# Kernel optimization log

Hardware: AMD Instinct MI355X
Metric: run time of the kernel (lower is better)

Reference implementation:

```python
import jax, jax.numpy as jnp
import numpy as np

NUM_SAMPLES = 512
FG_FRACTION = 0.25
MAX_POS = int(NUM_SAMPLES * FG_FRACTION)  # 128
THRESHOLDS = np.array([0.0, 0.5, 0.5], dtype=np.float32)
INDICATORS = np.array([-3, -1, -2, 1], dtype=np.int32)


def _make_boxes(key, shape, scale):
    # random valid boxes: sorted corner pairs in [0, scale)
    y = jnp.sort(jax.random.uniform(key, shape[:-1] + (2,)) * scale, axis=-1)
    x = jnp.sort(jax.random.uniform(jax.random.fold_in(key, 1), shape[:-1] + (2,)) * scale, axis=-1)
    return jnp.stack([y[..., 0], x[..., 0], y[..., 1], x[..., 1]], axis=-1)


def setup_inputs() -> dict:
    key = jax.random.key(0)
    k1, k2, k3, k4 = jax.random.split(key, 4)
    B, N, M = 32, 8000, 256
    boxes = _make_boxes(k1, (B, N, 4), 1024.0)
    gt_boxes = _make_boxes(k2, (B, M, 4), 1024.0)
    # pad last quarter of gt entries with -1 (invalid)
    valid = (jnp.arange(M) < (3 * M) // 4)[None, :, None]
    gt_boxes = jnp.where(valid, gt_boxes, -jnp.ones_like(gt_boxes))
    gt_classes = jax.random.randint(k3, (B, M), 1, 91, dtype=jnp.int32)
    gt_classes = jnp.where(valid[..., 0], gt_classes, -1)
    rand = jax.random.uniform(k4, (B, N + M))
    return {"boxes": boxes, "gt_boxes": gt_boxes, "gt_classes": gt_classes, "rand": rand}


def _pairwise_iou(b1, b2):
    # b1: [B,N,4], b2: [B,M,4] in (ymin,xmin,ymax,xmax) -> [B,N,M]
    ymin1, xmin1, ymax1, xmax1 = jnp.split(b1, 4, axis=-1)  # each [B,N,1]
    ymin2, xmin2, ymax2, xmax2 = (t[..., 0] for t in jnp.split(b2, 4, axis=-1))  # [B,M]
    ih = jnp.clip(jnp.minimum(ymax1, ymax2[:, None, :]) - jnp.maximum(ymin1, ymin2[:, None, :]), 0.0)
    iw = jnp.clip(jnp.minimum(xmax1, xmax2[:, None, :]) - jnp.maximum(xmin1, xmin2[:, None, :]), 0.0)
    inter = ih * iw
    a1 = (ymax1 - ymin1) * (xmax1 - xmin1)          # [B,N,1]
    a2 = (ymax2 - ymin2) * (xmax2 - xmin2)          # [B,M]
    union = a1 + a2[:, None, :] - inter
    return jnp.where(union > 0, inter / union, 0.0)


def _ranks_desc(score):
    order = jnp.argsort(-score)
    return jnp.zeros_like(order).at[order].set(jnp.arange(score.shape[0]))


def _sample_one(pos, neg, ign, rand):
    cand = (pos | neg) & ~ign
    pos_c = pos & cand
    neg_c = neg & cand
    pos_rank = _ranks_desc(jnp.where(pos_c, rand, -1.0))
    pos_sel = pos_c & (pos_rank < MAX_POS)
    neg_needed = NUM_SAMPLES - jnp.sum(pos_sel)
    neg_rank = _ranks_desc(jnp.where(neg_c, rand, -1.0))
    neg_sel = neg_c & (neg_rank < neg_needed)
    indicator = (pos_sel | neg_sel).astype(jnp.int32)
    _, idx = jax.lax.top_k(indicator, NUM_SAMPLES)  # selected first, ties by lowest index
    return idx


def _gather(t, idx):
    # t: [B,L,C], idx: [B,K] -> [B,K,C]
    return jnp.take_along_axis(t, idx[..., None], axis=1)


def reference(boxes, gt_boxes, gt_classes, rand):
    gt_boxes = gt_boxes.astype(boxes.dtype)
    boxes = jnp.concatenate([boxes, gt_boxes], axis=1)  # mix_gt_boxes
    boxes_invalid = jnp.max(boxes, axis=-1) < 0.0       # [B,L]
    gt_invalid = jnp.max(gt_boxes, axis=-1) < 0.0       # [B,M]
    sim = _pairwise_iou(boxes, gt_boxes)                # [B,L,M]
    sim = jnp.where(boxes_invalid[:, :, None] | gt_invalid[:, None, :], -1.0, sim)

    matched_vals = jnp.max(sim, axis=-1)                # [B,L]
    matched_gt_indices = jnp.argmax(sim, axis=-1).astype(jnp.int32)
    bucket = jnp.searchsorted(jnp.asarray(THRESHOLDS), matched_vals, side='right')
    match_indicators = jnp.asarray(INDICATORS)[bucket]  # [B,L]

    positive = match_indicators >= 0
    negative = match_indicators == -1
    ignored = match_indicators == -2
    invalid = match_indicators == -3
    background = negative | invalid                     # [B,L]

    matched_gt_classes = _gather(gt_classes[..., None], matched_gt_indices)[..., 0]
    matched_gt_classes = jnp.where(background, 0, matched_gt_classes)
    matched_gt_boxes = _gather(gt_boxes, matched_gt_indices)
    matched_gt_boxes = jnp.where(background[..., None], 0.0, matched_gt_boxes)
    matched_gt_indices = jnp.where(background, -1, matched_gt_indices)

    indices = jax.vmap(_sample_one)(positive, negative, ignored, rand)  # [B,K]
    rois = _gather(boxes, indices)
    sampled_gt_boxes = _gather(matched_gt_boxes, indices)
    sampled_gt_classes = _gather(matched_gt_classes[..., None], indices)[..., 0]
    sampled_gt_indices = _gather(matched_gt_indices[..., None], indices)[..., 0]
    return rois, sampled_gt_boxes, sampled_gt_classes, sampled_gt_indices
```

## Files before the change

### kernel.cpp

```cpp
#include <hip/hip_runtime.h>
#include <stdint.h>

#define BB 32
#define NN 8000
#define MM 256
#define LL (NN + MM)
#define NSAMP 512
#define MAXPOS 128
#define T2 1024
#define CH ((LL + T2 - 1) / T2)
#define SPLIT 4
#define MSUB (MM / SPLIT)
#define MARGIN 1.9073486328125e-06f

__device__ __forceinline__ void opaquef(float& x) { asm("" : "+v"(x)); }

__global__ __launch_bounds__(256) void match_split_kernel(
    const float* __restrict__ boxes, const float* __restrict__ gt,
    uint8_t* __restrict__ pidx)
{
    __shared__ float4 s_gt[MSUB];
    __shared__ float  s_a2[MSUB];
    const int b = blockIdx.y, sp = blockIdx.z, tid = threadIdx.x;
    if (tid < MSUB) {
        float4 v = ((const float4*)(gt + ((size_t)b * MM + sp * MSUB) * 4))[tid];
        s_gt[tid] = v;
        s_a2[tid] = (v.z - v.x) * (v.w - v.y);
    }
    __syncthreads();
    const int l = blockIdx.x * 256 + tid;
    if (l >= LL) return;

    float4 bx = (l < NN) ? ((const float4*)(boxes + (size_t)b * NN * 4))[l]
                         : ((const float4*)(gt + (size_t)b * MM * 4))[l - NN];
    int lbidx = 0;
    if (!(fmaxf(fmaxf(bx.x, bx.y), fmaxf(bx.z, bx.w)) < 0.0f)) {
        float a1 = (bx.z - bx.x) * (bx.w - bx.y);
        opaquef(a1);
        float bI0 = 0.f, bI1 = 0.f, bI2 = 0.f, bI3 = 0.f;
        float bS0 = 1.f, bS1 = 1.f, bS2 = 1.f, bS3 = 1.f;
        int bi0 = 0, bi1 = 1, bi2 = 2, bi3 = 3;
        bool redo = false;
        #pragma unroll 4
        for (int m = 0; m < MSUB; m += 4) {
            #define CHAIN_STEP(K, BI, BS, BIX)                                   \
            {                                                                    \
                float4 g = s_gt[m + K];                                          \
                float ih = fmaxf(fminf(bx.z, g.z) - fmaxf(bx.x, g.x), 0.0f);     \
                float iw = fmaxf(fminf(bx.w, g.w) - fmaxf(bx.y, g.y), 0.0f);     \
                float inter = ih * iw; opaquef(inter);                           \
                float s  = a1 + s_a2[m + K];                                     \
                float p1 = inter * BS, p2 = BI * s;                              \
                float d  = p1 - p2;                                              \
                float t  = MARGIN * fmaxf(p1, p2);                               \
                redo |= (fabsf(d) < t + t);                                      \
                if (d > t) { BI = inter; BS = s; BIX = m + K; }                  \
            }
            CHAIN_STEP(0, bI0, bS0, bi0)
            CHAIN_STEP(1, bI1, bS1, bi1)
            CHAIN_STEP(2, bI2, bS2, bi2)
            CHAIN_STEP(3, bI3, bS3, bi3)
            #undef CHAIN_STEP
        }
        float bbI = bI0, bbS = bS0; int bbi = bi0;
        #define CHAIN_MERGE(BI, BS, BIX)                                         \
        {                                                                        \
            float p1 = BI * bbS, p2 = bbI * BS;                                  \
            float d  = p1 - p2;                                                  \
            float t  = MARGIN * fmaxf(p1, p2);                                   \
            redo |= (fabsf(d) < t + t);                                          \
            if (d > t) { bbI = BI; bbS = BS; bbi = BIX; }                        \
        }
        CHAIN_MERGE(bI1, bS1, bi1)
        CHAIN_MERGE(bI2, bS2, bi2)
        CHAIN_MERGE(bI3, bS3, bi3)
        #undef CHAIN_MERGE
        lbidx = bbi;
        if (redo) {
            float qb = -1.0f; int bi = 0;
            for (int m = 0; m < MSUB; ++m) {
                float4 g = s_gt[m];
                float ih = fmaxf(fminf(bx.z, g.z) - fmaxf(bx.x, g.x), 0.0f);
                float iw = fmaxf(fminf(bx.w, g.w) - fmaxf(bx.y, g.y), 0.0f);
                float inter = ih * iw; opaquef(inter);
                float uni = (a1 + s_a2[m]) - inter;
                float q = (uni > 0.0f) ? (inter / uni) : 0.0f;
                if (q > qb) { qb = q; bi = m; }
            }
            lbidx = bi;
        }
    }
    pidx[((size_t)b * LL + l) * SPLIT + sp] = (uint8_t)lbidx;
}

__global__ __launch_bounds__(256) void merge_kernel(
    const float* __restrict__ boxes, const float* __restrict__ gt,
    const uint8_t* __restrict__ pidx, uint16_t* __restrict__ packed)
{
    const int b = blockIdx.y;
    const int l = blockIdx.x * 256 + threadIdx.x;
    if (l >= LL) return;
    float4 bx = (l < NN) ? ((const float4*)(boxes + (size_t)b * NN * 4))[l]
                         : ((const float4*)(gt + (size_t)b * MM * 4))[l - NN];
    int cls, bidx = 0;
    if (fmaxf(fmaxf(bx.x, bx.y), fmaxf(bx.z, bx.w)) < 0.0f) {
        cls = 2;
    } else {
        float a1 = (bx.z - bx.x) * (bx.w - bx.y);
        opaquef(a1);
        float qb = -1.0f;
        const uint32_t pv = *(const uint32_t*)&pidx[((size_t)b * LL + l) * SPLIT];
        #pragma unroll
        for (int sp = 0; sp < SPLIT; ++sp) {
            const int m = sp * MSUB + (int)((pv >> (8 * sp)) & 0xFFu);
            float4 g = ((const float4*)(gt + (size_t)b * MM * 4))[m];
            float a2 = (g.z - g.x) * (g.w - g.y); opaquef(a2);
            float ih = fmaxf(fminf(bx.z, g.z) - fmaxf(bx.x, g.x), 0.0f);
            float iw = fmaxf(fminf(bx.w, g.w) - fmaxf(bx.y, g.y), 0.0f);
            float inter = ih * iw; opaquef(inter);
            float uni = (a1 + a2) - inter;
            float q = (uni > 0.0f) ? (inter / uni) : 0.0f;
            if (q > qb) { qb = q; bidx = m; }
        }
        cls = (qb >= 0.5f) ? 1 : 0;
    }
    packed[(size_t)b * LL + l] = (uint16_t)(cls | (bidx << 2));
}

__device__ __forceinline__ int block_exscan_fast(int v, int* wt, int tid)
{
    const int lane = tid & 63, w = tid >> 6;
    int x = v;
    #pragma unroll
    for (int off = 1; off < 64; off <<= 1) {
        int y = __shfl_up(x, off);
        if (lane >= off) x += y;
    }
    if (lane == 63) wt[w] = x;
    __syncthreads();
    if (tid < 64) {
        int t = (tid < 16) ? wt[tid] : 0;
        #pragma unroll
        for (int off = 1; off < 16; off <<= 1) {
            int y = __shfl_up(t, off);
            if (tid >= off) t += y;
        }
        if (tid < 16) wt[tid] = t;
    }
    __syncthreads();
    return ((w > 0) ? wt[w - 1] : 0) + x - v;
}

__device__ __forceinline__ int block_exscan_seg4(int v, int* wt, int tid)
{
    const int lane = tid & 63, w = tid >> 6;
    int x = v;
    #pragma unroll
    for (int off = 1; off < 64; off <<= 1) {
        int y = __shfl_up(x, off);
        if (lane >= off) x += y;
    }
    if (lane == 63) wt[w] = x;
    __syncthreads();
    if (tid < 16) {
        int t = wt[tid];
        #pragma unroll
        for (int off = 1; off < 4; off <<= 1) {
            int y = __shfl_up(t, off);
            if ((tid & 3) >= off) t += y;
        }
        wt[tid] = t;
    }
    __syncthreads();
    return (((w & 3) > 0) ? wt[w - 1] : 0) + x - v;
}

__global__ __launch_bounds__(T2) void sample_kernel(
    const float* __restrict__ boxes, const float* __restrict__ gt,
    const int* __restrict__ gtc, const float* __restrict__ rnd,
    const uint16_t* __restrict__ packed, float* __restrict__ out)
{
    __shared__ uint32_t s_key[LL];
    __shared__ uint16_t s_pk[LL];
    __shared__ int s_hist[512];
    __shared__ int s_warp[16];
    __shared__ int s_idx[NSAMP];
    __shared__ int s_sb[8];
    const int b = blockIdx.x, tid = threadIdx.x, lane = tid & 63;

    if (tid == 0) s_sb[0] = 0;
    __syncthreads();

    int loc = 0;
    for (int l = tid; l < LL; l += T2) {
        s_key[l] = __float_as_uint(rnd[(size_t)b * LL + l]);
        uint16_t p = packed[(size_t)b * LL + l];
        s_pk[l] = p;
        int c = p & 3;
        loc += (c == 0) ? 1 : ((c == 1) ? 0x10000 : 0);
    }
    #pragma unroll
    for (int off = 32; off; off >>= 1) loc += __shfl_xor(loc, off);
    if (lane == 0) atomicAdd(&s_sb[0], loc);
    __syncthreads();
    const int Nn = s_sb[0] & 0xFFFF, P = s_sb[0] >> 16;

    const int posK = (P < MAXPOS) ? P : MAXPOS;
    const int negK = NSAMP - posK;
    const bool negRad = (Nn > negK);
    const bool posRad = (P > MAXPOS);

    uint32_t prefix0 = 0, prefix1 = 0;
    int rem0 = negK, rem1 = MAXPOS;
    if (negRad || posRad) {
        for (int round = 0; round < 4; ++round) {
            const int shift = 24 - 8 * round;
            if (tid < 512) s_hist[tid] = 0;
            __syncthreads();
            const uint32_t pmask = (round == 0) ? 0u : (0xFFFFFFFFu << (shift + 8));
            for (int l = tid; l < LL; l += T2) {
                const uint32_t k = s_key[l];
                const int c = s_pk[l] & 3;
                bool doit = (c == 0) ? (negRad && ((k & pmask) == prefix0))
                          : (c == 1) ? (posRad && ((k & pmask) == prefix1))
                          : false;
                if (doit) atomicAdd(&s_hist[(c << 8) | ((k >> shift) & 255)], 1);
            }
            __syncthreads();
            int h = 0;
            if (tid < 512) h = s_hist[(tid & 0x100) | (255 - (tid & 255))];
            const int above = block_exscan_seg4(h, s_warp, tid);
            if (tid < 512) {
                const int c = tid >> 8;
                const int rem = c ? rem1 : rem0;
                const bool act = c ? posRad : negRad;
                if (act && above < rem && above + h >= rem) {
                    s_sb[4 + c * 2] = 255 - (tid & 255);
                    s_sb[5 + c * 2] = above;
                }
            }
            __syncthreads();
            if (negRad) { prefix0 |= ((uint32_t)s_sb[4]) << shift; rem0 -= s_sb[5]; }
            if (posRad) { prefix1 |= ((uint32_t)s_sb[6]) << shift; rem1 -= s_sb[7]; }
            __syncthreads();
        }
    }
    const uint32_t thr0 = negRad ? prefix0 : 0u;  const int r0 = negRad ? rem0 : LL;
    const uint32_t thr1 = posRad ? prefix1 : 0u;  const int r1 = posRad ? rem1 : LL;

    const int lo = tid * CH, hi = (lo + CH < LL) ? (lo + CH) : LL;
    int nt = 0;
    for (int l = lo; l < hi; ++l) {
        const int c = s_pk[l] & 3;
        const uint32_t k = s_key[l];
        if (c == 0) { if (k == thr0) nt += 1; }
        else if (c == 1) { if (k == thr1) nt += 0x10000; }
    }
    const int basep = block_exscan_fast(nt, s_warp, tid);
    int base0 = basep & 0xFFFF, base1 = basep >> 16;
    for (int l = lo; l < hi; ++l) {
        const int c = s_pk[l] & 3;
        if (c > 1) continue;
        const uint32_t k = s_key[l];
        const uint32_t thr = c ? thr1 : thr0;
        bool sel = (k > thr);
        if (k == thr) {
            if (c == 0) { sel = (base0 < r0); ++base0; }
            else        { sel = (base1 < r1); ++base1; }
        }
        if (sel) s_pk[l] |= 0x8000;
    }
    __syncthreads();

    int cnt = 0;
    for (int l = lo; l < hi; ++l) cnt += (s_pk[l] & 0x8000) ? 1 : 0x10000;
    const int pb = block_exscan_fast(cnt, s_warp, tid);
    const int S = s_warp[15] & 0xFFFF;
    int bs = pb & 0xFFFF, bu = (pb >> 16) + S;
    for (int l = lo; l < hi; ++l) {
        if (s_pk[l] & 0x8000) { if (bs < NSAMP) s_idx[bs] = l; ++bs; }
        else                  { if (bu < NSAMP) s_idx[bu] = l; ++bu; }
    }
    __syncthreads();

    if (tid < NSAMP) {
        const int l = s_idx[tid];
        float4 bx = (l < NN) ? ((const float4*)(boxes + (size_t)b * NN * 4))[l]
                             : ((const float4*)(gt + (size_t)b * MM * 4))[l - NN];
        const int p = s_pk[l];
        const int c = p & 3, mi = (p >> 2) & 0xFF;
        const bool bg = (c != 1);
        float4 gb = make_float4(0.f, 0.f, 0.f, 0.f);
        int cl = 0, si = -1;
        if (!bg) {
            gb = ((const float4*)(gt + (size_t)b * MM * 4))[mi];
            cl = gtc[(size_t)b * MM + mi];
            si = mi;
        }
        const size_t rk = (size_t)b * NSAMP + tid;
        ((float4*)out)[rk] = bx;
        ((float4*)(out + (size_t)BB * NSAMP * 4))[rk] = gb;
        out[(size_t)2 * BB * NSAMP * 4 + rk] = (float)cl;
        out[(size_t)2 * BB * NSAMP * 4 + (size_t)BB * NSAMP + rk] = (float)si;
    }
}

extern "C" void kernel_launch(void* const* d_in, const int* in_sizes, int n_in,
                              void* d_out, int out_size, void* d_ws, size_t ws_size,
                              hipStream_t stream)
{
    const float* boxes = (const float*)d_in[0];
    const float* gt    = (const float*)d_in[1];
    const int*   gtc   = (const int*)  d_in[2];
    const float* rnd   = (const float*)d_in[3];
    float* out = (float*)d_out;
    uint8_t*  pidx   = (uint8_t*)d_ws;
    uint16_t* packed = (uint16_t*)((char*)d_ws + (size_t)BB * LL * SPLIT);

    dim3 g1((LL + 255) / 256, BB, SPLIT);
    match_split_kernel<<<g1, 256, 0, stream>>>(boxes, gt, pidx);
    dim3 g2((LL + 255) / 256, BB);
    merge_kernel<<<g2, 256, 0, stream>>>(boxes, gt, pidx, packed);
    sample_kernel<<<BB, T2, 0, stream>>>(boxes, gt, gtc, rnd, packed, out);
}
```

Baseline: 73.33 us.

## Fuse merge into sample kernel and process two boxes per thread in matching

Drops the separate merge kernel and does the per-split argmax merge and classification inside the sample kernel's load loop, saving a launch and the packed round trip through global memory. The match kernel now handles two boxes per thread, so each shared-memory ground-truth load is reused twice. The tie-margin test is rewritten with multiplicative bounds, and the serial fallback is moved into a non-inlined function behind a wave-wide any check. The merge work now runs on only 32 blocks in the sample kernel, which may serialise it. The match kernel also gets fewer threads in flight.

```diff
diff --git a/kernel.cpp b/kernel.cpp
--- a/kernel.cpp
+++ b/kernel.cpp
@@ -11,9 +11,26 @@
 #define CH ((LL + T2 - 1) / T2)
 #define SPLIT 4
 #define MSUB (MM / SPLIT)
-#define MARGIN 1.9073486328125e-06f
+#define ONE_P 1.0000019073486328f
+#define ONE_M 0.9999980926513672f
 
 __device__ __forceinline__ void opaquef(float& x) { asm("" : "+v"(x)); }
+
+__device__ __noinline__ int serial_argmax(const float4 bx, const float a1,
+                                          const float4* s_gt, const float* s_a2)
+{
+    float qb = -1.0f; int bi = 0;
+    for (int m = 0; m < MSUB; ++m) {
+        float4 g = s_gt[m];
+        float ih = fmaxf(fminf(bx.z, g.z) - fmaxf(bx.x, g.x), 0.0f);
+        float iw = fmaxf(fminf(bx.w, g.w) - fmaxf(bx.y, g.y), 0.0f);
+        float inter = ih * iw; opaquef(inter);
+        float uni = (a1 + s_a2[m]) - inter;
+        float q = (uni > 0.0f) ? (inter / uni) : 0.0f;
+        if (q > qb) { qb = q; bi = m; }
+    }
+    return bi;
+}
 
 __global__ __launch_bounds__(256) void match_split_kernel(
     const float* __restrict__ boxes, const float* __restrict__ gt,
@@ -28,103 +45,65 @@
         s_a2[tid] = (v.z - v.x) * (v.w - v.y);
     }
     __syncthreads();
-    const int l = blockIdx.x * 256 + tid;
-    if (l >= LL) return;
-
-    float4 bx = (l < NN) ? ((const float4*)(boxes + (size_t)b * NN * 4))[l]
-                         : ((const float4*)(gt + (size_t)b * MM * 4))[l - NN];
-    int lbidx = 0;
-    if (!(fmaxf(fmaxf(bx.x, bx.y), fmaxf(bx.z, bx.w)) < 0.0f)) {
-        float a1 = (bx.z - bx.x) * (bx.w - bx.y);
-        opaquef(a1);
-        float bI0 = 0.f, bI1 = 0.f, bI2 = 0.f, bI3 = 0.f;
-        float bS0 = 1.f, bS1 = 1.f, bS2 = 1.f, bS3 = 1.f;
-        int bi0 = 0, bi1 = 1, bi2 = 2, bi3 = 3;
-        bool redo = false;
-        #pragma unroll 4
-        for (int m = 0; m < MSUB; m += 4) {
-            #define CHAIN_STEP(K, BI, BS, BIX)                                   \
-            {                                                                    \
-                float4 g = s_gt[m + K];                                          \
-                float ih = fmaxf(fminf(bx.z, g.z) - fmaxf(bx.x, g.x), 0.0f);     \
-                float iw = fmaxf(fminf(bx.w, g.w) - fmaxf(bx.y, g.y), 0.0f);     \
-                float inter = ih * iw; opaquef(inter);                           \
-                float s  = a1 + s_a2[m + K];                                     \
-                float p1 = inter * BS, p2 = BI * s;                              \
-                float d  = p1 - p2;                                              \
-                float t  = MARGIN * fmaxf(p1, p2);                               \
-                redo |= (fabsf(d) < t + t);                                      \
-                if (d > t) { BI = inter; BS = s; BIX = m + K; }                  \
-            }
-            CHAIN_STEP(0, bI0, bS0, bi0)
-            CHAIN_STEP(1, bI1, bS1, bi1)
-            CHAIN_STEP(2, bI2, bS2, bi2)
-            CHAIN_STEP(3, bI3, bS3, bi3)
-            #undef CHAIN_STEP
-        }
-        float bbI = bI0, bbS = bS0; int bbi = bi0;
-        #define CHAIN_MERGE(BI, BS, BIX)                                         \
-        {                                                                        \
-            float p1 = BI * bbS, p2 = bbI * BS;                                  \
-            float d  = p1 - p2;                                                  \
-            float t  = MARGIN * fmaxf(p1, p2);                                   \
-            redo |= (fabsf(d) < t + t);                                          \
-            if (d > t) { bbI = BI; bbS = BS; bbi = BIX; }                        \
-        }
-        CHAIN_MERGE(bI1, bS1, bi1)
-        CHAIN_MERGE(bI2, bS2, bi2)
-        CHAIN_MERGE(bI3, bS3, bi3)
-        #undef CHAIN_MERGE
-        lbidx = bbi;
-        if (redo) {
-            float qb = -1.0f; int bi = 0;
-            for (int m = 0; m < MSUB; ++m) {
-                float4 g = s_gt[m];
-                float ih = fmaxf(fminf(bx.z, g.z) - fmaxf(bx.x, g.x), 0.0f);
-                float iw = fmaxf(fminf(bx.w, g.w) - fmaxf(bx.y, g.y), 0.0f);
-                float inter = ih * iw; opaquef(inter);
-                float uni = (a1 + s_a2[m]) - inter;
-                float q = (uni > 0.0f) ? (inter / uni) : 0.0f;
-                if (q > qb) { qb = q; bi = m; }
-            }
-            lbidx = bi;
-        }
-    }
-    pidx[((size_t)b * LL + l) * SPLIT + sp] = (uint8_t)lbidx;
-}
-
-__global__ __launch_bounds__(256) void merge_kernel(
-    const float* __restrict__ boxes, const float* __restrict__ gt,
-    const uint8_t* __restrict__ pidx, uint16_t* __restrict__ packed)
-{
-    const int b = blockIdx.y;
-    const int l = blockIdx.x * 256 + threadIdx.x;
-    if (l >= LL) return;
-    float4 bx = (l < NN) ? ((const float4*)(boxes + (size_t)b * NN * 4))[l]
-                         : ((const float4*)(gt + (size_t)b * MM * 4))[l - NN];
-    int cls, bidx = 0;
-    if (fmaxf(fmaxf(bx.x, bx.y), fmaxf(bx.z, bx.w)) < 0.0f) {
-        cls = 2;
-    } else {
-        float a1 = (bx.z - bx.x) * (bx.w - bx.y);
-        opaquef(a1);
-        float qb = -1.0f;
-        const uint32_t pv = *(const uint32_t*)&pidx[((size_t)b * LL + l) * SPLIT];
-        #pragma unroll
-        for (int sp = 0; sp < SPLIT; ++sp) {
-            const int m = sp * MSUB + (int)((pv >> (8 * sp)) & 0xFFu);
-            float4 g = ((const float4*)(gt + (size_t)b * MM * 4))[m];
-            float a2 = (g.z - g.x) * (g.w - g.y); opaquef(a2);
-            float ih = fmaxf(fminf(bx.z, g.z) - fmaxf(bx.x, g.x), 0.0f);
-            float iw = fmaxf(fminf(bx.w, g.w) - fmaxf(bx.y, g.y), 0.0f);
-            float inter = ih * iw; opaquef(inter);
-            float uni = (a1 + a2) - inter;
-            float q = (uni > 0.0f) ? (inter / uni) : 0.0f;
-            if (q > qb) { qb = q; bidx = m; }
-        }
-        cls = (qb >= 0.5f) ? 1 : 0;
-    }
-    packed[(size_t)b * LL + l] = (uint16_t)(cls | (bidx << 2));
+    const int l0 = blockIdx.x * 512 + tid * 2;
+    if (l0 >= LL) return;
+    const int l1 = l0 + 1;
+    const bool v1 = (l1 < LL);
+    const int l1c = v1 ? l1 : l0;
+
+    const float4* bb4 = (const float4*)(boxes + (size_t)b * NN * 4);
+    const float4* gb4 = (const float4*)(gt + (size_t)b * MM * 4);
+    float4 bx0 = (l0 < NN) ? bb4[l0] : gb4[l0 - NN];
+    float4 bx1 = (l1c < NN) ? bb4[l1c] : gb4[l1c - NN];
+
+    float a10 = (bx0.z - bx0.x) * (bx0.w - bx0.y); opaquef(a10);
+    float a11 = (bx1.z - bx1.x) * (bx1.w - bx1.y); opaquef(a11);
+
+    float I00 = 0.f, S00 = 1.f, I01 = 0.f, S01 = 1.f;
+    float I10 = 0.f, S10 = 1.f, I11 = 0.f, S11 = 1.f;
+    int X00 = 0, X01 = 1, X10 = 0, X11 = 1;
+    bool redo0 = false, redo1 = false;
+
+    #define STEP(BX, A1, G, A2, BI, BS, BIX, MIDX, RD)                       \
+    {                                                                        \
+        float ih = fmaxf(fminf(BX.z, G.z) - fmaxf(BX.x, G.x), 0.0f);         \
+        float iw = fmaxf(fminf(BX.w, G.w) - fmaxf(BX.y, G.y), 0.0f);         \
+        float inter = ih * iw; opaquef(inter);                               \
+        float s  = A1 + A2;                                                  \
+        float p1 = inter * BS, p2 = BI * s;                                  \
+        bool win = p1 > p2 * ONE_P;                                          \
+        RD |= ((p1 > p2 * ONE_M) != win);                                    \
+        if (win) { BI = inter; BS = s; BIX = MIDX; }                         \
+    }
+    #pragma unroll 4
+    for (int m = 0; m < MSUB; m += 2) {
+        float4 g0 = s_gt[m];     float a2_0 = s_a2[m];
+        float4 g1 = s_gt[m + 1]; float a2_1 = s_a2[m + 1];
+        STEP(bx0, a10, g0, a2_0, I00, S00, X00, m,     redo0)
+        STEP(bx0, a10, g1, a2_1, I01, S01, X01, m + 1, redo0)
+        STEP(bx1, a11, g0, a2_0, I10, S10, X10, m,     redo1)
+        STEP(bx1, a11, g1, a2_1, I11, S11, X11, m + 1, redo1)
+    }
+    #undef STEP
+
+    #define MERGE(I0, S0, X0, I1, S1, X1, RD)                                \
+    {                                                                        \
+        float p1 = I1 * S0, p2 = I0 * S1;                                    \
+        bool win = p1 > p2 * ONE_P;                                          \
+        RD |= ((p1 > p2 * ONE_M) != win);                                    \
+        if (win) { X0 = X1; }                                                \
+    }
+    MERGE(I00, S00, X00, I01, S01, X01, redo0)
+    MERGE(I10, S10, X10, I11, S11, X11, redo1)
+    #undef MERGE
+
+    int lb0 = X00, lb1 = X10;
+    if (__any(redo0 || redo1)) {
+        if (redo0) lb0 = serial_argmax(bx0, a10, s_gt, s_a2);
+        if (redo1) lb1 = serial_argmax(bx1, a11, s_gt, s_a2);
+    }
+    pidx[((size_t)b * LL + l0) * SPLIT + sp] = (uint8_t)lb0;
+    if (v1) pidx[((size_t)b * LL + l1) * SPLIT + sp] = (uint8_t)lb1;
 }
 
 __device__ __forceinline__ int block_exscan_fast(int v, int* wt, int tid)
@@ -178,7 +157,7 @@
 __global__ __launch_bounds__(T2) void sample_kernel(
     const float* __restrict__ boxes, const float* __restrict__ gt,
     const int* __restrict__ gtc, const float* __restrict__ rnd,
-    const uint16_t* __restrict__ packed, float* __restrict__ out)
+    const uint32_t* __restrict__ pidx, float* __restrict__ out)
 {
     __shared__ uint32_t s_key[LL];
     __shared__ uint16_t s_pk[LL];
@@ -187,6 +166,8 @@
     __shared__ int s_idx[NSAMP];
     __shared__ int s_sb[8];
     const int b = blockIdx.x, tid = threadIdx.x, lane = tid & 63;
+    const float4* bb4 = (const float4*)(boxes + (size_t)b * NN * 4);
+    const float4* gb4 = (const float4*)(gt + (size_t)b * MM * 4);
 
     if (tid == 0) s_sb[0] = 0;
     __syncthreads();
@@ -194,10 +175,28 @@
     int loc = 0;
     for (int l = tid; l < LL; l += T2) {
         s_key[l] = __float_as_uint(rnd[(size_t)b * LL + l]);
-        uint16_t p = packed[(size_t)b * LL + l];
-        s_pk[l] = p;
-        int c = p & 3;
-        loc += (c == 0) ? 1 : ((c == 1) ? 0x10000 : 0);
+        const uint32_t pv = pidx[(size_t)b * LL + l];
+        float4 bx = (l < NN) ? bb4[l] : gb4[l - NN];
+        int cls = 2, midx = 0;
+        if (!(fmaxf(fmaxf(bx.x, bx.y), fmaxf(bx.z, bx.w)) < 0.0f)) {
+            float a1 = (bx.z - bx.x) * (bx.w - bx.y); opaquef(a1);
+            float qb = -1.0f;
+            #pragma unroll
+            for (int sp = 0; sp < SPLIT; ++sp) {
+                const int m = sp * MSUB + (int)((pv >> (8 * sp)) & 0xFFu);
+                float4 g = gb4[m];
+                float a2 = (g.z - g.x) * (g.w - g.y); opaquef(a2);
+                float ih = fmaxf(fminf(bx.z, g.z) - fmaxf(bx.x, g.x), 0.0f);
+                float iw = fmaxf(fminf(bx.w, g.w) - fmaxf(bx.y, g.y), 0.0f);
+                float inter = ih * iw; opaquef(inter);
+                float uni = (a1 + a2) - inter;
+                float q = (uni > 0.0f) ? (inter / uni) : 0.0f;
+                if (q > qb) { qb = q; midx = m; }
+            }
+            cls = (qb >= 0.5f) ? 1 : 0;
+        }
+        s_pk[l] = (uint16_t)(cls | (midx << 2));
+        loc += (cls == 0) ? 1 : ((cls == 1) ? 0x10000 : 0);
     }
     #pragma unroll
     for (int off = 32; off; off >>= 1) loc += __shfl_xor(loc, off);
@@ -285,15 +284,14 @@
 
     if (tid < NSAMP) {
         const int l = s_idx[tid];
-        float4 bx = (l < NN) ? ((const float4*)(boxes + (size_t)b * NN * 4))[l]
-                             : ((const float4*)(gt + (size_t)b * MM * 4))[l - NN];
+        float4 bx = (l < NN) ? bb4[l] : gb4[l - NN];
         const int p = s_pk[l];
         const int c = p & 3, mi = (p >> 2) & 0xFF;
         const bool bg = (c != 1);
         float4 gb = make_float4(0.f, 0.f, 0.f, 0.f);
         int cl = 0, si = -1;
         if (!bg) {
-            gb = ((const float4*)(gt + (size_t)b * MM * 4))[mi];
+            gb = gb4[mi];
             cl = gtc[(size_t)b * MM + mi];
             si = mi;
         }
@@ -314,12 +312,10 @@
     const int*   gtc   = (const int*)  d_in[2];
     const float* rnd   = (const float*)d_in[3];
     float* out = (float*)d_out;
-    uint8_t*  pidx   = (uint8_t*)d_ws;
-    uint16_t* packed = (uint16_t*)((char*)d_ws + (size_t)BB * LL * SPLIT);
-
-    dim3 g1((LL + 255) / 256, BB, SPLIT);
+    uint8_t* pidx = (uint8_t*)d_ws;
+
+    dim3 g1((LL + 511) / 512, BB, SPLIT);
     match_split_kernel<<<g1, 256, 0, stream>>>(boxes, gt, pidx);
-    dim3 g2((LL + 255) / 256, BB);
-    merge_kernel<<<g2, 256, 0, stream>>>(boxes, gt, pidx, packed);
-    sample_kernel<<<BB, T2, 0, stream>>>(boxes, gt, gtc, rnd, packed, out);
-}
+    sample_kernel<<<BB, T2, 0, stream>>>(boxes, gt, gtc, rnd,
+                                         (const uint32_t*)d_ws, out);
+}
```

Measured after the change: 74.32 us. About the same (+1.4%).

## Register-block IoU matching with packed-key argmax and approximate reciprocal

Applied to the files above, without the earlier changes.

The split matching kernel now has each thread handle four boxes, so each shared-memory GT load is reused across them. The per-pair cross-multiplied comparison chains are replaced by an approximate IoU proxy, inter times the reciprocal of the area sum. It is packed with the GT index into a uint32 key, with a max for the best and a max-of-min for the runner-up. A near-tie check on the top two keys falls back to the exact serial argmax, which moves into a noinline function. This cuts per-pair ALU work and the grid size, but it raises register pressure, lowers the wave count, and the tie detection relies on a heuristic quantization margin.

```diff
diff --git a/kernel.cpp b/kernel.cpp
--- a/kernel.cpp
+++ b/kernel.cpp
@@ -11,9 +11,25 @@
 #define CH ((LL + T2 - 1) / T2)
 #define SPLIT 4
 #define MSUB (MM / SPLIT)
-#define MARGIN 1.9073486328125e-06f
+#define BPT 4
 
 __device__ __forceinline__ void opaquef(float& x) { asm("" : "+v"(x)); }
+
+__device__ __noinline__ int serial_argmax(const float4 bx, const float a1,
+                                          const float4* s_gt, const float* s_a2)
+{
+    float qb = -1.0f; int bi = 0;
+    for (int m = 0; m < MSUB; ++m) {
+        float4 g = s_gt[m];
+        float ih = fmaxf(fminf(bx.z, g.z) - fmaxf(bx.x, g.x), 0.0f);
+        float iw = fmaxf(fminf(bx.w, g.w) - fmaxf(bx.y, g.y), 0.0f);
+        float inter = ih * iw; opaquef(inter);
+        float uni = (a1 + s_a2[m]) - inter;
+        float q = (uni > 0.0f) ? (inter / uni) : 0.0f;
+        if (q > qb) { qb = q; bi = m; }
+    }
+    return bi;
+}
 
 __global__ __launch_bounds__(256) void match_split_kernel(
     const float* __restrict__ boxes, const float* __restrict__ gt,
@@ -28,69 +44,59 @@
         s_a2[tid] = (v.z - v.x) * (v.w - v.y);
     }
     __syncthreads();
-    const int l = blockIdx.x * 256 + tid;
-    if (l >= LL) return;
-
-    float4 bx = (l < NN) ? ((const float4*)(boxes + (size_t)b * NN * 4))[l]
-                         : ((const float4*)(gt + (size_t)b * MM * 4))[l - NN];
-    int lbidx = 0;
-    if (!(fmaxf(fmaxf(bx.x, bx.y), fmaxf(bx.z, bx.w)) < 0.0f)) {
-        float a1 = (bx.z - bx.x) * (bx.w - bx.y);
-        opaquef(a1);
-        float bI0 = 0.f, bI1 = 0.f, bI2 = 0.f, bI3 = 0.f;
-        float bS0 = 1.f, bS1 = 1.f, bS2 = 1.f, bS3 = 1.f;
-        int bi0 = 0, bi1 = 1, bi2 = 2, bi3 = 3;
-        bool redo = false;
-        #pragma unroll 4
-        for (int m = 0; m < MSUB; m += 4) {
-            #define CHAIN_STEP(K, BI, BS, BIX)                                   \
-            {                                                                    \
-                float4 g = s_gt[m + K];                                          \
-                float ih = fmaxf(fminf(bx.z, g.z) - fmaxf(bx.x, g.x), 0.0f);     \
-                float iw = fmaxf(fminf(bx.w, g.w) - fmaxf(bx.y, g.y), 0.0f);     \
-                float inter = ih * iw; opaquef(inter);                           \
-                float s  = a1 + s_a2[m + K];                                     \
-                float p1 = inter * BS, p2 = BI * s;                              \
-                float d  = p1 - p2;                                              \
-                float t  = MARGIN * fmaxf(p1, p2);                               \
-                redo |= (fabsf(d) < t + t);                                      \
-                if (d > t) { BI = inter; BS = s; BIX = m + K; }                  \
-            }
-            CHAIN_STEP(0, bI0, bS0, bi0)
-            CHAIN_STEP(1, bI1, bS1, bi1)
-            CHAIN_STEP(2, bI2, bS2, bi2)
-            CHAIN_STEP(3, bI3, bS3, bi3)
-            #undef CHAIN_STEP
-        }
-        float bbI = bI0, bbS = bS0; int bbi = bi0;
-        #define CHAIN_MERGE(BI, BS, BIX)                                         \
-        {                                                                        \
-            float p1 = BI * bbS, p2 = bbI * BS;                                  \
-            float d  = p1 - p2;                                                  \
-            float t  = MARGIN * fmaxf(p1, p2);                                   \
-            redo |= (fabsf(d) < t + t);                                          \
-            if (d > t) { bbI = BI; bbS = BS; bbi = BIX; }                        \
-        }
-        CHAIN_MERGE(bI1, bS1, bi1)
-        CHAIN_MERGE(bI2, bS2, bi2)
-        CHAIN_MERGE(bI3, bS3, bi3)
-        #undef CHAIN_MERGE
-        lbidx = bbi;
-        if (redo) {
-            float qb = -1.0f; int bi = 0;
-            for (int m = 0; m < MSUB; ++m) {
-                float4 g = s_gt[m];
-                float ih = fmaxf(fminf(bx.z, g.z) - fmaxf(bx.x, g.x), 0.0f);
-                float iw = fmaxf(fminf(bx.w, g.w) - fmaxf(bx.y, g.y), 0.0f);
-                float inter = ih * iw; opaquef(inter);
-                float uni = (a1 + s_a2[m]) - inter;
-                float q = (uni > 0.0f) ? (inter / uni) : 0.0f;
-                if (q > qb) { qb = q; bi = m; }
-            }
-            lbidx = bi;
-        }
-    }
-    pidx[((size_t)b * LL + l) * SPLIT + sp] = (uint8_t)lbidx;
+    const int l0 = blockIdx.x * (256 * BPT) + tid * BPT;
+    if (l0 >= LL) return;
+
+    const float4* bb4 = (const float4*)(boxes + (size_t)b * NN * 4);
+    const float4* gb4 = (const float4*)(gt + (size_t)b * MM * 4);
+
+    float4 bx[BPT]; float a1[BPT]; bool val[BPT];
+    uint32_t best[BPT], best2[BPT];
+    #pragma unroll
+    for (int j = 0; j < BPT; ++j) {
+        const int l = l0 + j;
+        val[j] = (l < LL);
+        const int lc = val[j] ? l : l0;
+        bx[j] = (lc < NN) ? bb4[lc] : gb4[lc - NN];
+        a1[j] = (bx[j].z - bx[j].x) * (bx[j].w - bx[j].y);
+        best[j] = 0; best2[j] = 0;
+    }
+
+    #pragma unroll 8
+    for (int m = 0; m < MSUB; ++m) {
+        const float4 g = s_gt[m];
+        const float a2 = s_a2[m];
+        #pragma unroll
+        for (int j = 0; j < BPT; ++j) {
+            float ih = fmaxf(fminf(bx[j].z, g.z) - fmaxf(bx[j].x, g.x), 0.0f);
+            float iw = fmaxf(fminf(bx[j].w, g.w) - fmaxf(bx[j].y, g.y), 0.0f);
+            float inter = ih * iw;
+            float s = fmaxf(a1[j] + a2, 1e-30f);
+            float u = inter * __builtin_amdgcn_rcpf(s);
+            uint32_t key = (__float_as_uint(u) & 0xFFFFFFC0u) | (uint32_t)(63 - m);
+            uint32_t old = best[j];
+            best[j]  = max(old, key);
+            best2[j] = max(best2[j], min(old, key));
+        }
+    }
+
+    int lb[BPT]; bool redo[BPT]; bool anyredo = false;
+    #pragma unroll
+    for (int j = 0; j < BPT; ++j) {
+        lb[j] = 63 - (int)(best[j] & 63u);
+        const uint32_t qp = best[j] & 0xFFFFFFC0u;
+        redo[j] = val[j] && (qp != 0u) &&
+                  ((qp - (best2[j] & 0xFFFFFFC0u)) <= 64u);
+        anyredo |= redo[j];
+    }
+    if (__any(anyredo)) {
+        #pragma unroll
+        for (int j = 0; j < BPT; ++j)
+            if (redo[j]) lb[j] = serial_argmax(bx[j], a1[j], s_gt, s_a2);
+    }
+    #pragma unroll
+    for (int j = 0; j < BPT; ++j)
+        if (val[j]) pidx[((size_t)b * LL + (l0 + j)) * SPLIT + sp] = (uint8_t)lb[j];
 }
 
 __global__ __launch_bounds__(256) void merge_kernel(
@@ -187,6 +193,8 @@
     __shared__ int s_idx[NSAMP];
     __shared__ int s_sb[8];
     const int b = blockIdx.x, tid = threadIdx.x, lane = tid & 63;
+    const float4* bb4 = (const float4*)(boxes + (size_t)b * NN * 4);
+    const float4* gb4 = (const float4*)(gt + (size_t)b * MM * 4);
 
     if (tid == 0) s_sb[0] = 0;
     __syncthreads();
@@ -285,15 +293,14 @@
 
     if (tid < NSAMP) {
         const int l = s_idx[tid];
-        float4 bx = (l < NN) ? ((const float4*)(boxes + (size_t)b * NN * 4))[l]
-                             : ((const float4*)(gt + (size_t)b * MM * 4))[l - NN];
+        float4 bx = (l < NN) ? bb4[l] : gb4[l - NN];
         const int p = s_pk[l];
         const int c = p & 3, mi = (p >> 2) & 0xFF;
         const bool bg = (c != 1);
         float4 gb = make_float4(0.f, 0.f, 0.f, 0.f);
         int cl = 0, si = -1;
         if (!bg) {
-            gb = ((const float4*)(gt + (size_t)b * MM * 4))[mi];
+            gb = gb4[mi];
             cl = gtc[(size_t)b * MM + mi];
             si = mi;
         }
@@ -317,7 +324,7 @@
     uint8_t*  pidx   = (uint8_t*)d_ws;
     uint16_t* packed = (uint16_t*)((char*)d_ws + (size_t)BB * LL * SPLIT);
 
-    dim3 g1((LL + 255) / 256, BB, SPLIT);
+    dim3 g1((LL + 256 * BPT - 1) / (256 * BPT), BB, SPLIT);
     match_split_kernel<<<g1, 256, 0, stream>>>(boxes, gt, pidx);
     dim3 g2((LL + 255) / 256, BB);
     merge_kernel<<<g2, 256, 0, stream>>>(boxes, gt, pidx, packed);
```

Result: slower. 79.02 us (+7.8%).
